# Performance work log

Hardware: AMD Instinct MI355X
Metric: run time of the kernel (lower is better)

The kernel has to match this reference:

```python
import jax, jax.numpy as jnp
import numpy as np

EPS = 1e-20
TEMP = 0.07
PATCH = 64
STEP = 32  # patch_size * overlap(0.5)


def zero_softmax(x, eps=1e-5):
    # ZeroSoftmax: ((exp(x)-1)^2) / (sum + eps), maps x==0 -> exactly 0 weight
    e = jnp.square(jnp.exp(x) - 1.0)
    return e / (jnp.sum(e, axis=-1, keepdims=True) + eps)


def _scaling_mask(H, W, p, step):
    # constant overlap-count mask from CRW.compute_scaling_mask (static shapes)
    sm = np.zeros((H, W), np.float32)
    for i in range(0, H - step, step):
        for j in range(0, W - step, step):
            sm[i:i + p, j:j + p] += 1.0
    return jnp.asarray(sm)


def _window_sums(m, p, step):
    # m: (B,T,SP,H,W) -> sliding-window sums (B,T,SP,nH,nW) via integral image
    ii = jnp.cumsum(jnp.cumsum(m, axis=-2), axis=-1)
    ii = jnp.pad(ii, ((0, 0), (0, 0), (0, 0), (1, 0), (1, 0)))
    H = m.shape[-2]
    nH = (H - p) // step + 1
    lo = jnp.arange(nH) * step
    hi = lo + p
    r_hi = ii[..., hi, :]   # (B,T,SP,nH,W+1)
    r_lo = ii[..., lo, :]
    return r_hi[..., hi] - r_hi[..., lo] - r_lo[..., hi] + r_lo[..., lo]


def setup_inputs() -> dict:
    key = jax.random.key(0)
    k1, k2, k3 = jax.random.split(key, 3)
    B, T, H, W = 2, 4, 256, 256
    nH = (H - PATCH) // STEP + 1  # 7
    N = nH * nH                   # 49 patches
    Cenc, D, SP = 512, 128, 64
    feats = jax.random.normal(k1, (B, N, Cenc, T), jnp.float32)
    W_head = jax.random.normal(k2, (Cenc, D), jnp.float32) / np.sqrt(Cenc)
    sp_mask = jax.random.randint(k3, (B, T, H, W), 0, SP, jnp.int32)
    return {"feats": feats, "W_head": W_head, "sp_mask": sp_mask, "max_sp_num": SP}


def reference(feats, W_head, sp_mask, max_sp_num):
    B, N, Cenc, T = feats.shape
    H, W = sp_mask.shape[-2:]
    SP = max_sp_num

    # --- pixels_to_nodes tail: projection head + L2 normalize over channel dim ---
    q = jnp.einsum('bnct,cd->bndt', feats, W_head)            # (B,N,128,T)
    nrm = jnp.maximum(jnp.linalg.norm(q, axis=2, keepdims=True), 1e-12)
    q = q / nrm
    q = jnp.transpose(q, (0, 2, 3, 1))                        # (B,128,T,N)

    # --- patches_to_sp_embeddings: windowed superpixel pooling ---
    oh = (sp_mask[:, :, None, :, :] ==
          jnp.arange(SP, dtype=sp_mask.dtype)[None, None, :, None, None]
          ).astype(jnp.float32)                               # (B,T,SP,H,W)
    sm = _scaling_mask(H, W, PATCH, STEP)                     # (H,W)
    ws = _window_sums(oh / sm, PATCH, STEP)                   # (B,T,SP,nH,nW)
    denom = jnp.sum(oh, axis=(-1, -2)) + EPS                  # (B,T,SP)
    wts = jnp.transpose(ws, (0, 1, 3, 4, 2)) / denom[:, :, None, None, :]
    wts = wts.reshape(B, T, N, SP)                            # (B,T,N,SP)
    q_sp = jnp.einsum('bdtn,btns->bdts', q, wts)              # (B,128,T,SP)

    # --- affinity + zero_softmax stochastic matrices ---
    As = jnp.einsum('bdtn,bdtm->btnm', q_sp[:, :, :-1], q_sp[:, :, 1:])  # (B,T-1,SP,SP)
    A12 = zero_softmax(As / TEMP)
    A21 = zero_softmax(jnp.swapaxes(As, -1, -2) / TEMP)

    # --- palindrome random walks + cross-entropy to cycle-consistency targets ---
    tgt = jnp.tile(jnp.arange(SP), B)
    loss = jnp.float32(0.0)
    AAs = []
    for i in range(1, T - 1):
        mats = [A12[:, k] for k in range(i + 1)] + [A21[:, k] for k in range(i, -1, -1)]
        aa = mats[0]
        for m in mats[1:]:
            aa = aa @ m
        AAs.append(aa)
        logits = jnp.log(aa + EPS).reshape(B * SP, SP)
        logp = jax.nn.log_softmax(logits, axis=-1)
        loss = loss + jnp.mean(-logp[jnp.arange(B * SP), tgt])
    return loss, jnp.stack(AAs)
```

## Files before the change

### kernel.cpp

```cpp
#include <hip/hip_runtime.h>
#include <hip/hip_bf16.h>

constexpr int NWIN = 49;
constexpr int QLD  = 52;

constexpr int OFF_WS   = 0;
constexpr int OFF_Q    = 26624;
constexpr int OFF_QSP  = 79872;
constexpr int OFF_A12  = 145408;
constexpr int OFF_A12T = 169984;
constexpr int OFF_A21  = 194560;
constexpr int OFF_A21T = 219136;
constexpr int OFF_P    = 243712;
constexpr int OFF_R1T  = 251904;
constexpr int OFF_L    = 260096;
constexpr int OFF_RT   = 268288;
constexpr int OFF_BAR  = 276480;

__global__ void __launch_bounds__(256, 1)
k_front(const int* __restrict__ mask, const float* __restrict__ feats,
        const float* __restrict__ Wh, float* __restrict__ ws, float* __restrict__ q) {
    if (blockIdx.x < 392) {
        int win = blockIdx.x % NWIN;
        int bt  = blockIdx.x / NWIN;
        int wy = win / 7, wx = win % 7;
        __shared__ float loc[64];
        if (threadIdx.x < 64) loc[threadIdx.x] = 0.f;
        __syncthreads();
        const int* base = mask + bt * 65536 + (wy * 32) * 256 + wx * 32;
        #pragma unroll
        for (int it = 0; it < 16; ++it) {
            int idx = it * 256 + (int)threadIdx.x;
            int r = idx >> 6, c = idx & 63;
            int s = base[r * 256 + c];
            int y = wy * 32 + r, x = wx * 32 + c;
            float w = 1.f;
            if (y >= 32 && y < 224) w *= 0.5f;
            if (x >= 32 && x < 224) w *= 0.5f;
            atomicAdd(&loc[s], w);
        }
        __syncthreads();
        if (threadIdx.x < 64) {
            ws[(bt * 64 + (int)threadIdx.x) * QLD + win] = loc[threadIdx.x];
        } else if (win == 0) {
            int s = threadIdx.x & 63;
            int col = 49 + (int)(threadIdx.x >> 6) - 1;
            ws[(bt * 64 + s) * QLD + col] = 0.f;
        }
    } else {
        int bid = blockIdx.x - 392;
        int n = bid % NWIN, b = bid / NWIN;
        __shared__ float4 f4[512];
        __shared__ float4 psum4[256];
        __shared__ float4 red4[2];
        const float4* fp4 = (const float4*)(feats + (size_t)(b * NWIN + n) * 2048);
        for (int i = threadIdx.x; i < 512; i += 256) f4[i] = fp4[i];
        __syncthreads();

        int d = threadIdx.x & 127, ch = threadIdx.x >> 7;
        float a0 = 0.f, a1 = 0.f, a2 = 0.f, a3 = 0.f;
        const float* wp = Wh + d;
        int c0 = ch * 256;
        #pragma unroll 8
        for (int c = c0; c < c0 + 256; ++c) {
            float w = wp[c * 128];
            float4 fv = f4[c];
            a0 += fv.x * w; a1 += fv.y * w; a2 += fv.z * w; a3 += fv.w * w;
        }
        psum4[threadIdx.x] = make_float4(a0, a1, a2, a3);
        __syncthreads();

        float4 A;
        if (threadIdx.x < 128) {
            float4 p0 = psum4[threadIdx.x], p1 = psum4[128 + threadIdx.x];
            A = make_float4(p0.x + p1.x, p0.y + p1.y, p0.z + p1.z, p0.w + p1.w);
            float sx = A.x * A.x, sy = A.y * A.y, sz = A.z * A.z, sw = A.w * A.w;
            for (int off = 32; off; off >>= 1) {
                sx += __shfl_down(sx, off); sy += __shfl_down(sy, off);
                sz += __shfl_down(sz, off); sw += __shfl_down(sw, off);
            }
            if ((threadIdx.x & 63) == 0) red4[threadIdx.x >> 6] = make_float4(sx, sy, sz, sw);
        }
        __syncthreads();
        if (threadIdx.x < 128) {
            float4 r0 = red4[0], r1 = red4[1];
            float ix = 1.f / fmaxf(sqrtf(r0.x + r1.x), 1e-12f);
            float iy = 1.f / fmaxf(sqrtf(r0.y + r1.y), 1e-12f);
            float iz = 1.f / fmaxf(sqrtf(r0.z + r1.z), 1e-12f);
            float iw = 1.f / fmaxf(sqrtf(r0.w + r1.w), 1e-12f);
            float* qb = q + (size_t)(b * 128 + d) * 4 * QLD + n;
            qb[0 * QLD] = A.x * ix;
            qb[1 * QLD] = A.y * iy;
            qb[2 * QLD] = A.z * iz;
            qb[3 * QLD] = A.w * iw;
        }
    }
}

__global__ void k_qsp(const float* __restrict__ q, const float* __restrict__ wsg,
                      float* __restrict__ qsp, float* __restrict__ out,
                      int* __restrict__ bar) {
    if (blockIdx.x == 0 && threadIdx.x < 4) {
        bar[threadIdx.x] = 0;
        if (threadIdx.x == 0) out[0] = 0.f;
    }
    int tid = blockIdx.x * 256 + threadIdx.x;
    int s = tid & 63;
    int d = (tid >> 6) & 127;
    int t = (tid >> 13) & 3;
    int b = tid >> 15;
    const float4* qrow = (const float4*)(q + (size_t)((b * 128 + d) * 4 + t) * QLD);
    const float4* wrow = (const float4*)(wsg + (size_t)((b * 4 + t) * 64 + s) * QLD);
    float acc = 0.f, den = 0.f;
    #pragma unroll
    for (int i = 0; i < 13; ++i) {
        float4 w = wrow[i];
        float4 qv = qrow[i];
        den += w.x + w.y + w.z + w.w;
        acc += qv.x * w.x + qv.y * w.y + qv.z * w.z + qv.w * w.w;
    }
    qsp[tid] = acc / (den + 1e-20f);
}


__device__ __forceinline__ void dump_mat(float* M, const float4* v) {
    #pragma unroll
    for (int it = 0; it < 4; ++it) {
        int idx = it * 256 + (int)threadIdx.x;
        int r = idx >> 4, c4 = (idx & 15) << 2;
        *(float4*)&M[r * 64 + (c4 ^ ((r & 15) << 2))] = v[it];
    }
}

__device__ __forceinline__ void stage2(float* Ma, float* Mb,
                                       const float* __restrict__ Ga,
                                       const float* __restrict__ Gb) {
    const float4* ga = (const float4*)Ga;
    const float4* gb = (const float4*)Gb;
    float4 va[4], vb[4];
    #pragma unroll
    for (int it = 0; it < 4; ++it) {
        int idx = it * 256 + (int)threadIdx.x;
        va[it] = ga[idx];
        vb[it] = gb[idx];
    }
    dump_mat(Ma, va);
    dump_mat(Mb, vb);
}

__device__ __forceinline__ void mm256_sw(float* acc, const float* Ra, const float* Rb) {
    int tid = threadIdx.x;
    int nl = tid >> 4, ml = tid & 15;
    int sxa = nl << 2, sxb = ml << 2;
    #pragma unroll
    for (int i = 0; i < 16; ++i) acc[i] = 0.f;
    #pragma unroll 4
    for (int k0 = 0; k0 < 64; k0 += 4) {
        float4 av[4], bv[4];
        #pragma unroll
        for (int i = 0; i < 4; ++i)
            av[i] = *(const float4*)&Ra[(nl + 16 * i) * 64 + (k0 ^ sxa)];
        #pragma unroll
        for (int j = 0; j < 4; ++j)
            bv[j] = *(const float4*)&Rb[(ml + 16 * j) * 64 + (k0 ^ sxb)];
        #pragma unroll
        for (int i = 0; i < 4; ++i)
            #pragma unroll
            for (int j = 0; j < 4; ++j)
                acc[i * 4 + j] += av[i].x * bv[j].x + av[i].y * bv[j].y
                                + av[i].z * bv[j].z + av[i].w * bv[j].w;
    }
}

__device__ __forceinline__ void store_mat(float* __restrict__ G, const float* acc) {
    int nl = threadIdx.x >> 4, ml = threadIdx.x & 15;
    #pragma unroll
    for (int i = 0; i < 4; ++i)
        #pragma unroll
        for (int j = 0; j < 4; ++j)
            G[(nl + 16 * i) * 64 + ml + 16 * j] = acc[i * 4 + j];
}

__device__ __forceinline__ void store_loss(const float* acc, float* __restrict__ aa,
                                           float* __restrict__ out, float* red) {
    int tid = threadIdx.x;
    int nl = tid >> 4, ml = tid & 15;
    #pragma unroll
    for (int i = 0; i < 4; ++i)
        #pragma unroll
        for (int j = 0; j < 4; ++j)
            aa[(nl + 16 * i) * 64 + (ml + 16 * j)] = acc[i * 4 + j];
    int l = tid & 63;
    float part = 0.f;
    #pragma unroll
    for (int i = 0; i < 4; ++i) {
        float rsum = acc[i * 4 + 0] + acc[i * 4 + 1] + acc[i * 4 + 2] + acc[i * 4 + 3];
        rsum += __shfl_down(rsum, 8, 16);
        rsum += __shfl_down(rsum, 4, 16);
        rsum += __shfl_down(rsum, 2, 16);
        rsum += __shfl_down(rsum, 1, 16);
        float dv = __shfl(acc[5 * i], (l & 48) | nl, 64);
        if ((l & 15) == 0) part += logf(rsum + 6.4e-19f) - logf(dv + 1e-20f);
    }
    for (int off = 32; off; off >>= 1) part += __shfl_down(part, off);
    if (l == 0) red[tid >> 6] = part;
    __syncthreads();
    if (tid == 0) atomicAdd(out, (red[0] + red[1] + red[2] + red[3]) * (1.f / 128.f));
}

__device__ __forceinline__ void gbar(int* cnt, int target) {
    __threadfence();
    __syncthreads();
    if (threadIdx.x == 0) {
        __hip_atomic_fetch_add(cnt, 1, __ATOMIC_ACQ_REL, __HIP_MEMORY_SCOPE_AGENT);
        while (__hip_atomic_load(cnt, __ATOMIC_ACQUIRE, __HIP_MEMORY_SCOPE_AGENT) < target)
            __builtin_amdgcn_s_sleep(2);
    }
    __syncthreads();
    __threadfence();
}

__global__ void __launch_bounds__(256, 1)
k_tail(const float* __restrict__ qsp,
       float* __restrict__ a12, float* __restrict__ a12T,
       float* __restrict__ a21, float* __restrict__ a21T,
       float* __restrict__ wsP, float* __restrict__ wsR1T,
       float* __restrict__ wsL, float* __restrict__ wsRT,
       float* __restrict__ out, int* __restrict__ bar) {
    __shared__ float SM[16384];
    const int tid = threadIdx.x;
    const int blk = blockIdx.x;

    {
        int t = blk % 3, b = blk / 3;
        float4* qaT4 = (float4*)SM;
        float4* qbT4 = (float4*)SM + 2048;
        {
            const float4* gA = (const float4*)(qsp + (size_t)(b * 4 + t) * 8192);
            const float4* gB = (const float4*)(qsp + (size_t)(b * 4 + t + 1) * 8192);
            float* qaF = (float*)qaT4;
            float* qbF = (float*)qbT4;
            #pragma unroll
            for (int it = 0; it < 8; ++it) {
                int idx = it * 256 + tid;
                int d = idx >> 4, s0 = (idx & 15) << 2;
                float4 va = gA[idx];
                float4 vb = gB[idx];
                int g = d >> 2, c = d & 3;
                #pragma unroll
                for (int u = 0; u < 4; ++u) {
                    int s = s0 + u;
                    int w = (s * 32 + (g ^ (s & 31))) * 4 + c;
                    float fa = (u == 0) ? va.x : (u == 1) ? va.y : (u == 2) ? va.z : va.w;
                    float fb = (u == 0) ? vb.x : (u == 1) ? vb.y : (u == 2) ? vb.z : vb.w;
                    qaF[w] = fa;
                    qbF[w] = fb;
                }
            }
        }
        __syncthreads();

        const int nl = tid >> 4, ml = tid & 15;
        float acc[16];
        #pragma unroll
        for (int i = 0; i < 16; ++i) acc[i] = 0.f;
        #pragma unroll 8
        for (int k4 = 0; k4 < 32; ++k4) {
            float4 av[4], bv[4];
            #pragma unroll
            for (int i = 0; i < 4; ++i) { int n = nl + 16 * i; av[i] = qaT4[n * 32 + (k4 ^ (n & 31))]; }
            #pragma unroll
            for (int j = 0; j < 4; ++j) { int m = ml + 16 * j; bv[j] = qbT4[m * 32 + (k4 ^ (m & 31))]; }
            #pragma unroll
            for (int i = 0; i < 4; ++i)
                #pragma unroll
                for (int j = 0; j < 4; ++j)
                    acc[i * 4 + j] += av[i].x * bv[j].x + av[i].y * bv[j].y
                                    + av[i].z * bv[j].z + av[i].w * bv[j].w;
        }
        __syncthreads();

        float* eb = (float*)qaT4;
        float* rs = (float*)qbT4;
        float* cs = rs + 64;
        #pragma unroll
        for (int i = 0; i < 4; ++i)
            #pragma unroll
            for (int j = 0; j < 4; ++j) {
                int n = nl + 16 * i, m = ml + 16 * j;
                float x = acc[i * 4 + j] * (1.f / 0.07f);
                float e = expf(x) - 1.f;
                eb[n * 65 + m] = e * e;
            }
        __syncthreads();
        if (tid < 128) {
            int r = tid & 63; bool isrow = tid < 64;
            float a = 0.f;
            #pragma unroll
            for (int k = 0; k < 64; ++k) a += isrow ? eb[r * 65 + k] : eb[k * 65 + r];
            (isrow ? rs : cs)[r] = a + 1e-5f;
        }
        __syncthreads();
        float* p12  = a12  + (b * 3 + t) * 4096;
        float* p12T = a12T + (b * 3 + t) * 4096;
        float* p21  = a21  + (b * 3 + t) * 4096;
        float* p21T = a21T + (b * 3 + t) * 4096;
        #pragma unroll
        for (int i = 0; i < 4; ++i)
            #pragma unroll
            for (int j = 0; j < 4; ++j) {
                int n = nl + 16 * i, m = ml + 16 * j;
                float v   = eb[n * 65 + m];
                float v12 = v / rs[n];
                float v21 = v / cs[m];
                if (t == 0) {
                    p12 [n * 64 + m] = v12;
                    p21T[n * 64 + m] = v21;
                } else {
                    p12T[m * 64 + n] = v12;
                    p21 [m * 64 + n] = v21;
                }
            }
    }
    gbar(bar + 0, 6);

    if (blk < 4) {
        int b = blk >> 1, which = blk & 1;
        float* Ma = SM;
        float* Mb = SM + 4096;
        if (which == 0) stage2(Ma, Mb, a12  + (b * 3 + 0) * 4096, a12T + (b * 3 + 1) * 4096);
        else            stage2(Ma, Mb, a21T + (b * 3 + 0) * 4096, a21  + (b * 3 + 1) * 4096);
        __syncthreads();
        float acc[16];
        mm256_sw(acc, Ma, Mb);
        store_mat((which == 0 ? wsP : wsR1T) + b * 4096, acc);
    }
    gbar(bar + 1, 6);

    {
        float* Ma = SM;
        float* Mb = SM + 4096;
        float* red = SM + 8192;
        if (blk < 2) {
            int b = blk;
            stage2(Ma, Mb, wsP + b * 4096, wsR1T + b * 4096);
            __syncthreads();
            float acc[16];
            mm256_sw(acc, Ma, Mb);
            store_loss(acc, out + 1 + b * 4096, out, red);
        } else if (blk < 4) {
            int b = blk - 2;
            stage2(Ma, Mb, wsP + b * 4096, a12T + (b * 3 + 2) * 4096);
            __syncthreads();
            float acc[16];
            mm256_sw(acc, Ma, Mb);
            store_mat(wsL + b * 4096, acc);
        } else {
            int b = blk - 4;
            stage2(Ma, Mb, wsR1T + b * 4096, a21 + (b * 3 + 2) * 4096);
            __syncthreads();
            float acc[16];
            mm256_sw(acc, Ma, Mb);
            store_mat(wsRT + b * 4096, acc);
        }
    }
    gbar(bar + 2, 6);

    if (blk < 2) {
        int b = blk;
        float* Ma = SM;
        float* Mb = SM + 4096;
        float* red = SM + 8192;
        stage2(Ma, Mb, wsL + b * 4096, wsRT + b * 4096);
        __syncthreads();
        float acc[16];
        mm256_sw(acc, Ma, Mb);
        store_loss(acc, out + 1 + (2 + b) * 4096, out, red);
    }
}

extern "C" void kernel_launch(void* const* d_in, const int* in_sizes, int n_in,
                              void* d_out, int out_size, void* d_ws, size_t ws_size,
                              hipStream_t stream) {
    const float* feats = (const float*)d_in[0];
    const float* Wh    = (const float*)d_in[1];
    const int*   mask  = (const int*)d_in[2];
    float* out = (float*)d_out;
    float* ws  = (float*)d_ws;

    float* ws_sums = ws + OFF_WS;
    float* q       = ws + OFF_Q;
    float* qsp     = ws + OFF_QSP;
    float* a12     = ws + OFF_A12;
    float* a12T    = ws + OFF_A12T;
    float* a21     = ws + OFF_A21;
    float* a21T    = ws + OFF_A21T;
    float* wsP     = ws + OFF_P;
    float* wsR1T   = ws + OFF_R1T;
    float* wsL     = ws + OFF_L;
    float* wsRT    = ws + OFF_RT;
    int*   bar     = (int*)(ws + OFF_BAR);

    k_front<<<392 + 2 * NWIN, 256, 0, stream>>>(mask, feats, Wh, ws_sums, q);
    k_qsp<<<256, 256, 0, stream>>>(q, ws_sums, qsp, out, bar);
    k_tail<<<6, 256, 0, stream>>>(qsp, a12, a12T, a21, a21T,
                                  wsP, wsR1T, wsL, wsRT, out, bar);
}
```

Baseline: 114.8 us.

## Fuse qsp pooling into tail kernel with grid barrier, drop feats LDS staging

```diff
diff --git a/kernel.cpp b/kernel.cpp
--- a/kernel.cpp
+++ b/kernel.cpp
@@ -19,8 +19,13 @@
 
 __global__ void __launch_bounds__(256, 1)
 k_front(const int* __restrict__ mask, const float* __restrict__ feats,
-        const float* __restrict__ Wh, float* __restrict__ ws, float* __restrict__ q) {
+        const float* __restrict__ Wh, float* __restrict__ ws, float* __restrict__ q,
+        float* __restrict__ out, int* __restrict__ bar) {
     if (blockIdx.x < 392) {
+        if (blockIdx.x == 0) {
+            if (threadIdx.x < 4) bar[threadIdx.x] = 0;
+            if (threadIdx.x == 4) out[0] = 0.f;
+        }
         int win = blockIdx.x % NWIN;
         int bt  = blockIdx.x / NWIN;
         int wy = win / 7, wx = win % 7;
@@ -50,12 +55,9 @@
     } else {
         int bid = blockIdx.x - 392;
         int n = bid % NWIN, b = bid / NWIN;
-        __shared__ float4 f4[512];
         __shared__ float4 psum4[256];
         __shared__ float4 red4[2];
         const float4* fp4 = (const float4*)(feats + (size_t)(b * NWIN + n) * 2048);
-        for (int i = threadIdx.x; i < 512; i += 256) f4[i] = fp4[i];
-        __syncthreads();
 
         int d = threadIdx.x & 127, ch = threadIdx.x >> 7;
         float a0 = 0.f, a1 = 0.f, a2 = 0.f, a3 = 0.f;
@@ -64,7 +66,7 @@
         #pragma unroll 8
         for (int c = c0; c < c0 + 256; ++c) {
             float w = wp[c * 128];
-            float4 fv = f4[c];
+            float4 fv = fp4[c];
             a0 += fv.x * w; a1 += fv.y * w; a2 += fv.z * w; a3 += fv.w * w;
         }
         psum4[threadIdx.x] = make_float4(a0, a1, a2, a3);
@@ -97,31 +99,6 @@
     }
 }
 
-__global__ void k_qsp(const float* __restrict__ q, const float* __restrict__ wsg,
-                      float* __restrict__ qsp, float* __restrict__ out,
-                      int* __restrict__ bar) {
-    if (blockIdx.x == 0 && threadIdx.x < 4) {
-        bar[threadIdx.x] = 0;
-        if (threadIdx.x == 0) out[0] = 0.f;
-    }
-    int tid = blockIdx.x * 256 + threadIdx.x;
-    int s = tid & 63;
-    int d = (tid >> 6) & 127;
-    int t = (tid >> 13) & 3;
-    int b = tid >> 15;
-    const float4* qrow = (const float4*)(q + (size_t)((b * 128 + d) * 4 + t) * QLD);
-    const float4* wrow = (const float4*)(wsg + (size_t)((b * 4 + t) * 64 + s) * QLD);
-    float acc = 0.f, den = 0.f;
-    #pragma unroll
-    for (int i = 0; i < 13; ++i) {
-        float4 w = wrow[i];
-        float4 qv = qrow[i];
-        den += w.x + w.y + w.z + w.w;
-        acc += qv.x * w.x + qv.y * w.y + qv.z * w.z + qv.w * w.w;
-    }
-    qsp[tid] = acc / (den + 1e-20f);
-}
-
 
 __device__ __forceinline__ void dump_mat(float* M, const float4* v) {
     #pragma unroll
@@ -220,16 +197,50 @@
     __threadfence();
 }
 
-__global__ void __launch_bounds__(256, 1)
-k_tail(const float* __restrict__ qsp,
-       float* __restrict__ a12, float* __restrict__ a12T,
-       float* __restrict__ a21, float* __restrict__ a21T,
-       float* __restrict__ wsP, float* __restrict__ wsR1T,
-       float* __restrict__ wsL, float* __restrict__ wsRT,
-       float* __restrict__ out, int* __restrict__ bar) {
+__global__ void __launch_bounds__(256, 2)
+k_tail2(const float* __restrict__ q, const float* __restrict__ wsg,
+        float* __restrict__ qsp,
+        float* __restrict__ a12, float* __restrict__ a12T,
+        float* __restrict__ a21, float* __restrict__ a21T,
+        float* __restrict__ wsP, float* __restrict__ wsR1T,
+        float* __restrict__ wsL, float* __restrict__ wsRT,
+        float* __restrict__ out, int* __restrict__ bar) {
     __shared__ float SM[16384];
     const int tid = threadIdx.x;
     const int blk = blockIdx.x;
+
+    {
+        int gid = blk * 256 + tid;
+        int s = gid & 63;
+        int d = (gid >> 6) & 127;
+        int t = (gid >> 13) & 3;
+        int b = gid >> 15;
+        const float4* qrow = (const float4*)(q + (size_t)((b * 128 + d) * 4 + t) * QLD);
+        const float4* wrow = (const float4*)(wsg + (size_t)((b * 4 + t) * 64 + s) * QLD);
+        float acc = 0.f, den = 0.f;
+        #pragma unroll
+        for (int i = 0; i < 13; ++i) {
+            float4 w = wrow[i];
+            float4 qv = qrow[i];
+            den += w.x + w.y + w.z + w.w;
+            acc += qv.x * w.x + qv.y * w.y + qv.z * w.z + qv.w * w.w;
+        }
+        qsp[gid] = acc / (den + 1e-20f);
+    }
+    __threadfence();
+    __syncthreads();
+    if (blk >= 6) {
+        if (tid == 0)
+            __hip_atomic_fetch_add(bar + 0, 1, __ATOMIC_ACQ_REL, __HIP_MEMORY_SCOPE_AGENT);
+        return;
+    }
+    if (tid == 0) {
+        __hip_atomic_fetch_add(bar + 0, 1, __ATOMIC_ACQ_REL, __HIP_MEMORY_SCOPE_AGENT);
+        while (__hip_atomic_load(bar + 0, __ATOMIC_ACQUIRE, __HIP_MEMORY_SCOPE_AGENT) < 256)
+            __builtin_amdgcn_s_sleep(2);
+    }
+    __syncthreads();
+    __threadfence();
 
     {
         int t = blk % 3, b = blk / 3;
@@ -322,7 +333,7 @@
                 }
             }
     }
-    gbar(bar + 0, 6);
+    gbar(bar + 1, 6);
 
     if (blk < 4) {
         int b = blk >> 1, which = blk & 1;
@@ -335,7 +346,7 @@
         mm256_sw(acc, Ma, Mb);
         store_mat((which == 0 ? wsP : wsR1T) + b * 4096, acc);
     }
-    gbar(bar + 1, 6);
+    gbar(bar + 2, 6);
 
     {
         float* Ma = SM;
@@ -364,7 +375,7 @@
             store_mat(wsRT + b * 4096, acc);
         }
     }
-    gbar(bar + 2, 6);
+    gbar(bar + 3, 6);
 
     if (blk < 2) {
         int b = blk;
@@ -401,8 +412,7 @@
     float* wsRT    = ws + OFF_RT;
     int*   bar     = (int*)(ws + OFF_BAR);
 
-    k_front<<<392 + 2 * NWIN, 256, 0, stream>>>(mask, feats, Wh, ws_sums, q);
-    k_qsp<<<256, 256, 0, stream>>>(q, ws_sums, qsp, out, bar);
-    k_tail<<<6, 256, 0, stream>>>(qsp, a12, a12T, a21, a21T,
-                                  wsP, wsR1T, wsL, wsRT, out, bar);
-}
+    k_front<<<392 + 2 * NWIN, 256, 0, stream>>>(mask, feats, Wh, ws_sums, q, out, bar);
+    k_tail2<<<256, 256, 0, stream>>>(q, ws_sums, qsp, a12, a12T, a21, a21T,
+                                     wsP, wsR1T, wsL, wsRT, out, bar);
+}
```

Measured after the change: 143.0 us. +24.5%, slower.

## Chain random-walk matmuls in LDS to cut grid barriers in tail kernel

Applied to the files above, without the earlier changes.

```diff
diff --git a/kernel.cpp b/kernel.cpp
--- a/kernel.cpp
+++ b/kernel.cpp
@@ -11,10 +11,8 @@
 constexpr int OFF_A12T = 169984;
 constexpr int OFF_A21  = 194560;
 constexpr int OFF_A21T = 219136;
-constexpr int OFF_P    = 243712;
 constexpr int OFF_R1T  = 251904;
 constexpr int OFF_L    = 260096;
-constexpr int OFF_RT   = 268288;
 constexpr int OFF_BAR  = 276480;
 
 __global__ void __launch_bounds__(256, 1)
@@ -132,6 +130,14 @@
     }
 }
 
+__device__ __forceinline__ void stage1(float* M, const float* __restrict__ G) {
+    const float4* g = (const float4*)G;
+    float4 v[4];
+    #pragma unroll
+    for (int it = 0; it < 4; ++it) v[it] = g[it * 256 + (int)threadIdx.x];
+    dump_mat(M, v);
+}
+
 __device__ __forceinline__ void stage2(float* Ma, float* Mb,
                                        const float* __restrict__ Ga,
                                        const float* __restrict__ Gb) {
@@ -170,6 +176,17 @@
                 acc[i * 4 + j] += av[i].x * bv[j].x + av[i].y * bv[j].y
                                 + av[i].z * bv[j].z + av[i].w * bv[j].w;
     }
+}
+
+__device__ __forceinline__ void wr256_sw(float* M, const float* acc) {
+    int nl = threadIdx.x >> 4, ml = threadIdx.x & 15;
+    #pragma unroll
+    for (int i = 0; i < 4; ++i)
+        #pragma unroll
+        for (int j = 0; j < 4; ++j) {
+            int r = nl + 16 * i, k = ml + 16 * j;
+            M[r * 64 + (((k & ~3) ^ ((r & 15) << 2)) | (k & 3))] = acc[i * 4 + j];
+        }
 }
 
 __device__ __forceinline__ void store_mat(float* __restrict__ G, const float* acc) {
@@ -224,10 +241,13 @@
 k_tail(const float* __restrict__ qsp,
        float* __restrict__ a12, float* __restrict__ a12T,
        float* __restrict__ a21, float* __restrict__ a21T,
-       float* __restrict__ wsP, float* __restrict__ wsR1T,
-       float* __restrict__ wsL, float* __restrict__ wsRT,
+       float* __restrict__ wsR1T, float* __restrict__ wsL,
        float* __restrict__ out, int* __restrict__ bar) {
     __shared__ float SM[16384];
+    float* M0 = SM;
+    float* M1 = SM + 4096;
+    float* M2 = SM + 8192;
+    float* M3 = SM + 12288;
     const int tid = threadIdx.x;
     const int blk = blockIdx.x;
 
@@ -323,59 +343,47 @@
             }
     }
     gbar(bar + 0, 6);
-
-    if (blk < 4) {
-        int b = blk >> 1, which = blk & 1;
-        float* Ma = SM;
-        float* Mb = SM + 4096;
-        if (which == 0) stage2(Ma, Mb, a12  + (b * 3 + 0) * 4096, a12T + (b * 3 + 1) * 4096);
-        else            stage2(Ma, Mb, a21T + (b * 3 + 0) * 4096, a21  + (b * 3 + 1) * 4096);
+    if (blk >= 4) return;
+
+    int b = blk >> 1, odd = blk & 1;
+    if (!odd) {
+        stage2(M0, M1, a12 + (b * 3 + 0) * 4096, a12T + (b * 3 + 1) * 4096);
         __syncthreads();
         float acc[16];
-        mm256_sw(acc, Ma, Mb);
-        store_mat((which == 0 ? wsP : wsR1T) + b * 4096, acc);
-    }
-    gbar(bar + 1, 6);
-
-    {
-        float* Ma = SM;
-        float* Mb = SM + 4096;
-        float* red = SM + 8192;
-        if (blk < 2) {
-            int b = blk;
-            stage2(Ma, Mb, wsP + b * 4096, wsR1T + b * 4096);
-            __syncthreads();
-            float acc[16];
-            mm256_sw(acc, Ma, Mb);
-            store_loss(acc, out + 1 + b * 4096, out, red);
-        } else if (blk < 4) {
-            int b = blk - 2;
-            stage2(Ma, Mb, wsP + b * 4096, a12T + (b * 3 + 2) * 4096);
-            __syncthreads();
-            float acc[16];
-            mm256_sw(acc, Ma, Mb);
-            store_mat(wsL + b * 4096, acc);
-        } else {
-            int b = blk - 4;
-            stage2(Ma, Mb, wsR1T + b * 4096, a21 + (b * 3 + 2) * 4096);
-            __syncthreads();
-            float acc[16];
-            mm256_sw(acc, Ma, Mb);
-            store_mat(wsRT + b * 4096, acc);
-        }
-    }
-    gbar(bar + 2, 6);
-
-    if (blk < 2) {
-        int b = blk;
-        float* Ma = SM;
-        float* Mb = SM + 4096;
-        float* red = SM + 8192;
-        stage2(Ma, Mb, wsL + b * 4096, wsRT + b * 4096);
+        mm256_sw(acc, M0, M1);
+        wr256_sw(M2, acc);
+        stage1(M3, a12T + (b * 3 + 2) * 4096);
+        __syncthreads();
+        float acc2[16];
+        mm256_sw(acc2, M2, M3);
+        store_mat(wsL + b * 4096, acc2);
+    } else {
+        stage2(M0, M1, a21T + (b * 3 + 0) * 4096, a21 + (b * 3 + 1) * 4096);
         __syncthreads();
         float acc[16];
-        mm256_sw(acc, Ma, Mb);
-        store_loss(acc, out + 1 + (2 + b) * 4096, out, red);
+        mm256_sw(acc, M0, M1);
+        store_mat(wsR1T + b * 4096, acc);
+        wr256_sw(M2, acc);
+        stage1(M3, a21 + (b * 3 + 2) * 4096);
+        __syncthreads();
+        float acc2[16];
+        mm256_sw(acc2, M2, M3);
+        wr256_sw(M1, acc2);
+    }
+    gbar(bar + 1, 4);
+
+    if (!odd) {
+        stage1(M3, wsR1T + b * 4096);
+        __syncthreads();
+        float acc[16];
+        mm256_sw(acc, M2, M3);
+        store_loss(acc, out + 1 + b * 4096, out, M0);
+    } else {
+        stage1(M0, wsL + b * 4096);
+        __syncthreads();
+        float acc[16];
+        mm256_sw(acc, M0, M1);
+        store_loss(acc, out + 1 + (2 + b) * 4096, out, M2);
     }
 }
 
@@ -395,14 +403,12 @@
     float* a12T    = ws + OFF_A12T;
     float* a21     = ws + OFF_A21;
     float* a21T    = ws + OFF_A21T;
-    float* wsP     = ws + OFF_P;
     float* wsR1T   = ws + OFF_R1T;
     float* wsL     = ws + OFF_L;
-    float* wsRT    = ws + OFF_RT;
     int*   bar     = (int*)(ws + OFF_BAR);
 
     k_front<<<392 + 2 * NWIN, 256, 0, stream>>>(mask, feats, Wh, ws_sums, q);
     k_qsp<<<256, 256, 0, stream>>>(q, ws_sums, qsp, out, bar);
     k_tail<<<6, 256, 0, stream>>>(qsp, a12, a12T, a21, a21T,
-                                  wsP, wsR1T, wsL, wsRT, out, bar);
-}
+                                  wsR1T, wsL, out, bar);
+}
```

After: 110.7 us. -3.6%, faster.
